# Kernel optimization log

Hardware: AMD Instinct MI355X
Metric: run time of the kernel (lower is better)

## Reference

```python
import math
import jax, jax.numpy as jnp
import numpy as np

N_HEAD = 16
STEP_DIM = 4


def _make_mask(T):
    # lower-triangular causal mask with every STEP_DIM-th column zeroed
    m = jnp.tril(jnp.ones((T, T), dtype=jnp.float32))
    cols = jnp.arange(T)
    keep_col = (cols % STEP_DIM) != (STEP_DIM - 1)
    return m * keep_col[None, :].astype(jnp.float32)  # [T, T]


def setup_inputs() -> dict:
    key = jax.random.key(0)
    ks = jax.random.split(key, 9)
    B, T, C = 2, 2048, 1024
    s = 1.0 / math.sqrt(C)
    return {
        "x": jax.random.normal(ks[0], (B, T, C), dtype=jnp.float32),
        "Wq": jax.random.normal(ks[1], (C, C), dtype=jnp.float32) * s,
        "bq": jnp.zeros((C,), dtype=jnp.float32),
        "Wk": jax.random.normal(ks[2], (C, C), dtype=jnp.float32) * s,
        "bk": jnp.zeros((C,), dtype=jnp.float32),
        "Wv": jax.random.normal(ks[3], (C, C), dtype=jnp.float32) * s,
        "bv": jnp.zeros((C,), dtype=jnp.float32),
        "Wp": jax.random.normal(ks[4], (C, C), dtype=jnp.float32) * s,
        "bp": jnp.zeros((C,), dtype=jnp.float32),
    }


def reference(x, Wq, bq, Wk, bk, Wv, bv, Wp, bp):
    B, T, C = x.shape
    H = N_HEAD
    D = C // H
    # QKV projections -> [B, H, T, D]
    def heads(y):
        return y.reshape(B, T, H, D).transpose(0, 2, 1, 3)
    q = heads(x @ Wq + bq)
    k = heads(x @ Wk + bk)
    v = heads(x @ Wv + bv)
    # scores [B, H, T, T]
    att = jnp.einsum("bhtd,bhsd->bhts", q, k) * (1.0 / math.sqrt(D))
    mask = _make_mask(T)  # [T, T]
    att = jnp.where(mask[None, None, :, :] == 0, -jnp.inf, att)
    att = jax.nn.softmax(att, axis=-1)
    y = jnp.einsum("bhts,bhsd->bhtd", att, v)  # [B, H, T, D]
    y = y.transpose(0, 2, 1, 3).reshape(B, T, C)
    return y @ Wp + bp
```

## Files before the change

### kernel.cpp

```cpp
#include <hip/hip_runtime.h>

typedef __bf16 bf16x8 __attribute__((ext_vector_type(8)));
typedef float  f32x4  __attribute__((ext_vector_type(4)));
typedef unsigned int u32x2 __attribute__((ext_vector_type(2)));
typedef unsigned short u16x8 __attribute__((ext_vector_type(8)));
typedef __attribute__((address_space(3))) const unsigned short* lds_cp;

#define T_SEQ 2048
#define C_DIM 1024
#define NH    16
#define HD    64
#define LOG2E 1.4426950408889634f

__device__ __forceinline__ unsigned short f2bf(float f) {
  unsigned u = __builtin_bit_cast(unsigned, f);
  u += 0x7FFFu + ((u >> 16) & 1u);
  return (unsigned short)(u >> 16);
}

__device__ __forceinline__ unsigned cvtpk(float lo, float hi) {
  unsigned r;
  asm("v_cvt_pk_bf16_f32 %0, %1, %2" : "=v"(r) : "v"(lo), "v"(hi));
  return r;
}

__device__ __forceinline__ bf16x8 tr_frag(lds_cp addr) {
  u32x2 lo, hi;
  asm volatile("ds_read_b64_tr_b16 %0, %2 offset:0\n\t"
               "ds_read_b64_tr_b16 %1, %2 offset:128"
               : "=&v"(lo), "=&v"(hi) : "v"(addr) : "memory");
  struct { u32x2 a, b; } s{lo, hi};
  return __builtin_bit_cast(bf16x8, s);
}

__device__ __forceinline__ void gload_lds16(const void* g, void* l) {
  __builtin_amdgcn_global_load_lds(
      (const __attribute__((address_space(1))) unsigned int*)g,
      (__attribute__((address_space(3))) unsigned int*)l, 16, 0, 0);
}

__global__ void k_cvt_x(const float* __restrict__ x, unsigned short* __restrict__ xb,
                        const float* __restrict__ bq, const float* __restrict__ bk,
                        const float* __restrict__ bv, float* __restrict__ bqkv) {
  const int bx = blockIdx.x;
  if (bx < 4096) {
    const int i = bx * 256 + threadIdx.x;
    const float4 v = ((const float4*)x)[i];
    ushort4 o;
    o.x = f2bf(v.x); o.y = f2bf(v.y); o.z = f2bf(v.z); o.w = f2bf(v.w);
    ((ushort4*)xb)[i] = o;
  } else {
    const int i = (bx - 4096) * 256 + threadIdx.x;
    bqkv[i] = (i < 1024) ? bq[i] : (i < 2048 ? bk[i - 1024] : bv[i - 2048]);
  }
}

__global__ void k_transpose_w(const float* __restrict__ Wq, const float* __restrict__ Wk,
                              const float* __restrict__ Wv, const float* __restrict__ Wp,
                              unsigned short* __restrict__ Wt,
                              unsigned short* __restrict__ Wpt) {
  __shared__ float tile[32][33];
  const int z = blockIdx.z;
  const float* W = (z == 0) ? Wq : (z == 1) ? Wk : (z == 2) ? Wv : Wp;
  unsigned short* D = (z < 3) ? (Wt + ((size_t)z << 20)) : Wpt;
  const int tx = threadIdx.x, ty = threadIdx.y;
  const int n0 = blockIdx.x * 32, k0 = blockIdx.y * 32;
#pragma unroll
  for (int i = 0; i < 32; i += 8)
    tile[ty + i][tx] = W[(size_t)(k0 + ty + i) * C_DIM + n0 + tx];
  __syncthreads();
#pragma unroll
  for (int i = 0; i < 32; i += 8)
    D[(size_t)(n0 + ty + i) * C_DIM + k0 + tx] = f2bf(tile[tx][ty + i]);
}

template<int KDIM>
__device__ __forceinline__ void gemm_tile_mainloop(
    const unsigned short* __restrict__ A,
    const unsigned short* __restrict__ Bt,
    int m0, int n0,
    unsigned short* As, unsigned short* Bs,
    f32x4 acc[4][4])
{
  const int tid  = threadIdx.x;
  const int lane = tid & 63;
  const int wave = tid >> 6;
  const int wr   = wave >> 1, wc = wave & 1;
  const int srow = lane >> 2;
  const int scol = (lane & 3) << 3;
  const int fr   = lane & 15, g = lane >> 4;

  const f32x4 zero = {0.f, 0.f, 0.f, 0.f};
#pragma unroll
  for (int m = 0; m < 4; ++m)
#pragma unroll
    for (int n = 0; n < 4; ++n) acc[m][n] = zero;

  const int nk = KDIM >> 5;
  for (int kt = 0; kt < nk; ++kt) {
    const int kb = kt << 5;
#pragma unroll
    for (int i = 0; i < 2; ++i) {
      const int c   = wave * 2 + i;
      const int row = c * 16 + srow;
      gload_lds16(A  + (size_t)(m0 + row) * KDIM + kb + scol, As + c * 512);
      gload_lds16(Bt + (size_t)(n0 + row) * KDIM + kb + scol, Bs + c * 512);
    }
    __syncthreads();
    bf16x8 af[4], bfr[4];
    const unsigned short* ap = As + (wr * 64 + fr) * 32 + g * 8;
    const unsigned short* bp = Bs + (wc * 64 + fr) * 32 + g * 8;
#pragma unroll
    for (int m = 0; m < 4; ++m) af[m]  = *(const bf16x8*)(ap + m * 512);
#pragma unroll
    for (int n = 0; n < 4; ++n) bfr[n] = *(const bf16x8*)(bp + n * 512);
#pragma unroll
    for (int m = 0; m < 4; ++m)
#pragma unroll
      for (int n = 0; n < 4; ++n)
        acc[m][n] = __builtin_amdgcn_mfma_f32_16x16x32_bf16(af[m], bfr[n], acc[m][n], 0, 0, 0);
    __syncthreads();
  }
}

__global__ __launch_bounds__(256) void k_gemm_qkv(
    const unsigned short* __restrict__ Xb,
    const unsigned short* __restrict__ Wt,
    const float* __restrict__ bias,
    unsigned short* __restrict__ Qb,
    unsigned short* __restrict__ Kb,
    unsigned short* __restrict__ Vt)
{
  __shared__ __attribute__((aligned(16))) unsigned short As[128 * 32];
  __shared__ __attribute__((aligned(16))) unsigned short Bs[128 * 32];
  f32x4 acc[4][4];
  const int bx  = blockIdx.x;
  const int xcd = bx & 7;
  const int jb  = bx >> 3;
  const int m0  = (xcd * 4 + (jb & 3)) * 128;
  const int n0  = (jb >> 2) * 128;
  gemm_tile_mainloop<1024>(Xb, Wt, m0, n0, As, Bs, acc);

  const int lane = threadIdx.x & 63, wave = threadIdx.x >> 6;
  const int wr = wave >> 1, wc = wave & 1;
  const int fr = lane & 15, g = lane >> 4;
  const int j = n0 >> 10;
#pragma unroll
  for (int ni = 0; ni < 4; ++ni) {
    const int col = n0 + wc * 64 + ni * 16 + fr;
    const int c = col & 1023, h = c >> 6, d = c & 63;
    const float bb = bias[col];
#pragma unroll
    for (int mi = 0; mi < 4; ++mi)
#pragma unroll
      for (int r = 0; r < 4; ++r) {
        const int row = m0 + wr * 64 + mi * 16 + g * 4 + r;
        const int b = row >> 11, t = row & 2047;
        const int bh = b * NH + h;
        const float v = acc[mi][ni][r] + bb;
        if (j == 0)      Qb[((size_t)bh * T_SEQ + t) * HD + d] = f2bf(v * (0.125f * LOG2E));
        else if (j == 1) Kb[((size_t)bh * T_SEQ + t) * HD + d] = f2bf(v);
        else             Vt[((size_t)bh * HD + d) * T_SEQ + t] =
                           ((t & 3) == 3) ? (unsigned short)0 : f2bf(v);
      }
  }
}

__global__ __launch_bounds__(128) void k_attn(
    const unsigned short* __restrict__ Qb,
    const unsigned short* __restrict__ Kb,
    const unsigned short* __restrict__ Vt,
    unsigned short* __restrict__ Yb)
{
  __shared__ __attribute__((aligned(128))) unsigned short Ks[2][64][64];
  __shared__ __attribute__((aligned(128))) unsigned short Vs[2][64][64];
  __shared__ __attribute__((aligned(128))) unsigned short Pc[2][2][64][16];

  const int i    = blockIdx.x;
  const int xcd  = i & 7;
  const int jj   = i >> 3;
  const int bh   = xcd * 4 + (jj & 3);
  const int qs   = jj >> 2;
  const int so   = qs >> 3;
  const int qtile = (so == 0) ? 31 - qs : (so == 1) ? qs - 8
                  : (so == 2) ? 39 - qs : qs - 16;
  const int lane  = threadIdx.x & 63;
  const int wave  = threadIdx.x >> 6;
  const int fr = lane & 15, g = lane >> 4;
  const int q0w = qtile * 64 + wave * 32;
  const int nt = qtile + 1;
  const size_t hbase = (size_t)bh * T_SEQ * HD;
  const unsigned short* Kh = Kb + hbase;
  const unsigned short* Vh = Vt + (size_t)bh * HD * T_SEQ;

  const int srow = lane >> 3;
  const int scol = ((lane & 7) ^ srow) << 3;
  const int frx  = (fr & 7) << 3;

  const unsigned short* qp = Qb + hbase + (size_t)(q0w + fr) * HD + g * 8;
  const bf16x8 qA0 = *(const bf16x8*)(qp);
  const bf16x8 qA1 = *(const bf16x8*)(qp + 32);
  const bf16x8 qB0 = *(const bf16x8*)(qp + 16 * HD);
  const bf16x8 qB1 = *(const bf16x8*)(qp + 16 * HD + 32);

  const u16x8 bo = {0x3F80u, 0x3F80u, 0x3F80u, 0u, 0x3F80u, 0x3F80u, 0x3F80u, 0u};
  const bf16x8 bones = __builtin_bit_cast(bf16x8, bo);

  const f32x4 zero = {0.f, 0.f, 0.f, 0.f};
  f32x4 yA[4], yB[4], lAcc, lBcc;
#pragma unroll
  for (int n = 0; n < 4; ++n) { yA[n] = zero; yB[n] = zero; }
  lAcc = zero; lBcc = zero;

  char* pwA = (char*)&Pc[wave][0][0][0] + fr * 32 + g * 8;
  char* pwB = (char*)&Pc[wave][1][0][0] + fr * 32 + g * 8;
  lds_cp trA = (lds_cp)(const unsigned short*)&Pc[wave][0][0][0] + fr * 4 + g * 128;
  lds_cp trB = (lds_cp)(const unsigned short*)&Pc[wave][1][0][0] + fr * 4 + g * 128;

  auto STAGE = [&](int buf, int s0) {
#pragma unroll
    for (int i2 = 0; i2 < 4; ++i2) {
      const int c = wave * 4 + i2;
      gload_lds16(Kh + (size_t)(s0 + c * 8 + srow) * HD + scol, &Ks[buf][c * 8][0]);
      gload_lds16(Vh + (size_t)(c * 8 + srow) * T_SEQ + s0 + scol, &Vs[buf][c * 8][0]);
    }
  };

  auto BODY = [&](int cur, int s0, bool diag) {
    bf16x8 kf[4][2];
#pragma unroll
    for (int n = 0; n < 4; ++n) {
      const unsigned short* kr = &Ks[cur][n * 16 + fr][0];
      kf[n][0] = *(const bf16x8*)(kr + ((g * 8) ^ frx));
      kf[n][1] = *(const bf16x8*)(kr + ((32 + g * 8) ^ frx));
    }
    f32x4 sA[4], sB[4];
#pragma unroll
    for (int n = 0; n < 4; ++n) {
      f32x4 a = zero, b = zero;
      a = __builtin_amdgcn_mfma_f32_16x16x32_bf16(qA0, kf[n][0], a, 0, 0, 0);
      a = __builtin_amdgcn_mfma_f32_16x16x32_bf16(qA1, kf[n][1], a, 0, 0, 0);
      b = __builtin_amdgcn_mfma_f32_16x16x32_bf16(qB0, kf[n][0], b, 0, 0, 0);
      b = __builtin_amdgcn_mfma_f32_16x16x32_bf16(qB1, kf[n][1], b, 0, 0, 0);
      sA[n] = a; sB[n] = b;
    }
    if (diag) {
#pragma unroll
      for (int n = 0; n < 4; ++n) {
        const int sc = s0 + n * 16 + fr;
#pragma unroll
        for (int r = 0; r < 4; ++r) {
          const int tA = q0w + g * 4 + r;
          sA[n][r] = (sc <= tA) ? sA[n][r] : -1e30f;
          sB[n][r] = (sc <= tA + 16) ? sB[n][r] : -1e30f;
        }
      }
    }
    bf16x8 vf[4][2];
#pragma unroll
    for (int n = 0; n < 4; ++n) {
      const unsigned short* vr = &Vs[cur][n * 16 + fr][0];
      vf[n][0] = *(const bf16x8*)(vr + ((g * 8) ^ frx));
      vf[n][1] = *(const bf16x8*)(vr + ((32 + g * 8) ^ frx));
    }
#pragma unroll
    for (int n = 0; n < 4; ++n) {
      u32x2 wa = {cvtpk(exp2f(sA[n][0]), exp2f(sA[n][1])),
                  cvtpk(exp2f(sA[n][2]), exp2f(sA[n][3]))};
      u32x2 wb = {cvtpk(exp2f(sB[n][0]), exp2f(sB[n][1])),
                  cvtpk(exp2f(sB[n][2]), exp2f(sB[n][3]))};
      *(u32x2*)(pwA + n * 512) = wa;
      *(u32x2*)(pwB + n * 512) = wb;
    }
    bf16x8 paA[2], paB[2];
    paA[0] = tr_frag(trA);       paA[1] = tr_frag(trA + 512);
    paB[0] = tr_frag(trB);       paB[1] = tr_frag(trB + 512);
    asm volatile("s_waitcnt lgkmcnt(0)" ::: "memory");
    __builtin_amdgcn_sched_barrier(0);
#pragma unroll
    for (int kk = 0; kk < 2; ++kk) {
#pragma unroll
      for (int n = 0; n < 4; ++n) {
        yA[n] = __builtin_amdgcn_mfma_f32_16x16x32_bf16(paA[kk], vf[n][kk], yA[n], 0, 0, 0);
        yB[n] = __builtin_amdgcn_mfma_f32_16x16x32_bf16(paB[kk], vf[n][kk], yB[n], 0, 0, 0);
      }
      lAcc = __builtin_amdgcn_mfma_f32_16x16x32_bf16(paA[kk], bones, lAcc, 0, 0, 0);
      lBcc = __builtin_amdgcn_mfma_f32_16x16x32_bf16(paB[kk], bones, lBcc, 0, 0, 0);
    }
  };

  STAGE(0, 0);
  __syncthreads();
  for (int t = 0; t < nt; ++t) {
    const int cur = t & 1;
    if (t + 1 < nt) STAGE(cur ^ 1, (t + 1) * 64);
    const int s0 = t * 64;
    BODY(cur, s0, s0 + 63 > q0w);
    __syncthreads();
  }

  const int b = bh >> 4, h = bh & 15;
#pragma unroll
  for (int r = 0; r < 4; ++r) {
    const float invA = 1.0f / lAcc[r], invB = 1.0f / lBcc[r];
    const int tA = q0w + g * 4 + r;
#pragma unroll
    for (int n = 0; n < 4; ++n) {
      Yb[((size_t)(b * T_SEQ + tA)) * C_DIM + h * HD + n * 16 + fr] = f2bf(yA[n][r] * invA);
      Yb[((size_t)(b * T_SEQ + tA + 16)) * C_DIM + h * HD + n * 16 + fr] = f2bf(yB[n][r] * invB);
    }
  }
}

__global__ __launch_bounds__(256) void k_gemm_out(
    const unsigned short* __restrict__ Yb,
    const unsigned short* __restrict__ Wpt,
    const float* __restrict__ bp,
    float* __restrict__ out)
{
  __shared__ __attribute__((aligned(16))) unsigned short As[128 * 32];
  __shared__ __attribute__((aligned(16))) unsigned short Bs[128 * 32];
  f32x4 acc[4][4];
  const int bx  = blockIdx.x;
  const int xcd = bx & 7;
  const int jb  = bx >> 3;
  const int m0  = (xcd * 4 + (jb & 3)) * 128;
  const int n0  = (jb >> 2) * 128;
  gemm_tile_mainloop<1024>(Yb, Wpt, m0, n0, As, Bs, acc);

  const int lane = threadIdx.x & 63, wave = threadIdx.x >> 6;
  const int wr = wave >> 1, wc = wave & 1;
  const int fr = lane & 15, g = lane >> 4;
#pragma unroll
  for (int ni = 0; ni < 4; ++ni) {
    const int col = n0 + wc * 64 + ni * 16 + fr;
    const float bb = bp[col];
#pragma unroll
    for (int mi = 0; mi < 4; ++mi)
#pragma unroll
      for (int r = 0; r < 4; ++r) {
        const int row = m0 + wr * 64 + mi * 16 + g * 4 + r;
        out[(size_t)row * C_DIM + col] = acc[mi][ni][r] + bb;
      }
  }
}

extern "C" void kernel_launch(void* const* d_in, const int* in_sizes, int n_in,
                              void* d_out, int out_size, void* d_ws, size_t ws_size,
                              hipStream_t stream) {
  const float* x  = (const float*)d_in[0];
  const float* Wq = (const float*)d_in[1];
  const float* bq = (const float*)d_in[2];
  const float* Wk = (const float*)d_in[3];
  const float* bk = (const float*)d_in[4];
  const float* Wv = (const float*)d_in[5];
  const float* bv = (const float*)d_in[6];
  const float* Wp = (const float*)d_in[7];
  const float* bp = (const float*)d_in[8];
  float* out = (float*)d_out;

  char* ws = (char*)d_ws;
  unsigned short* Xb   = (unsigned short*)(ws);
  unsigned short* Wt   = (unsigned short*)(ws + (8u  << 20));
  unsigned short* Wpt  = (unsigned short*)(ws + (14u << 20));
  float*          bqkv = (float*)         (ws + (16u << 20));
  unsigned short* Qb   = (unsigned short*)(ws + (16u << 20) + (64u << 10));
  unsigned short* Kb   = (unsigned short*)(ws + (24u << 20) + (64u << 10));
  unsigned short* Vt   = (unsigned short*)(ws + (32u << 20) + (64u << 10));
  unsigned short* Yb   = (unsigned short*)(ws + (40u << 20) + (64u << 10));

  k_cvt_x<<<4108, 256, 0, stream>>>(x, Xb, bq, bk, bv, bqkv);
  dim3 tb(32, 8);
  k_transpose_w<<<dim3(32, 32, 4), tb, 0, stream>>>(Wq, Wk, Wv, Wp, Wt, Wpt);
  k_gemm_qkv<<<dim3(768), 256, 0, stream>>>(Xb, Wt, bqkv, Qb, Kb, Vt);
  k_attn<<<dim3(1024), 128, 0, stream>>>(Qb, Kb, Vt, Yb);
  k_gemm_out<<<dim3(256), 256, 0, stream>>>(Yb, Wpt, bp, out);
}
```

Before: 130.9 us.

## Split long causal attention tiles across two KV halves and merge partials

Query tiles 16-31 are now processed by two blocks each, one per half of the KV range. Each block writes unnormalized fp32 partial outputs and row sums, and a new merge kernel adds the two partials and normalizes. The goal is to balance per-block work under the causal mask, so a few long tiles no longer set the tail. In exchange it adds an extra kernel launch, fp32 partial traffic to global memory, and relies on no running max being subtracted, so the partial sums can be added directly.

```diff
diff --git a/kernel.cpp b/kernel.cpp
--- a/kernel.cpp
+++ b/kernel.cpp
@@ -170,7 +170,9 @@
     const unsigned short* __restrict__ Qb,
     const unsigned short* __restrict__ Kb,
     const unsigned short* __restrict__ Vt,
-    unsigned short* __restrict__ Yb)
+    unsigned short* __restrict__ Yb,
+    float* __restrict__ Ypart,
+    float* __restrict__ Lpart)
 {
   __shared__ __attribute__((aligned(128))) unsigned short Ks[2][64][64];
   __shared__ __attribute__((aligned(128))) unsigned short Vs[2][64][64];
@@ -178,17 +180,20 @@
 
   const int i    = blockIdx.x;
   const int xcd  = i & 7;
-  const int jj   = i >> 3;
-  const int bh   = xcd * 4 + (jj & 3);
-  const int qs   = jj >> 2;
-  const int so   = qs >> 3;
-  const int qtile = (so == 0) ? 31 - qs : (so == 1) ? qs - 8
-                  : (so == 2) ? 39 - qs : qs - 16;
+  const int j    = i >> 3;
+  const int bh   = xcd * 4 + (j & 3);
+  const int u    = j >> 2;
+  const int gg   = u >> 3, vv0 = u & 7;
+  const int vv   = (gg & 1) ? 7 - vv0 : vv0;
+  int qtile, t0, t1, half;
+  if (gg < 2)      { qtile = (gg == 0 ? 16 : 24) + vv; t0 = 0; t1 = (qtile + 1) >> 1; half = 0; }
+  else if (gg < 4) { qtile = (gg == 2 ? 16 : 24) + vv; t0 = (qtile + 1) >> 1; t1 = qtile + 1; half = 1; }
+  else             { qtile = (gg == 4 ? 0 : 8) + vv;   t0 = 0; t1 = qtile + 1; half = -1; }
+
   const int lane  = threadIdx.x & 63;
   const int wave  = threadIdx.x >> 6;
   const int fr = lane & 15, g = lane >> 4;
   const int q0w = qtile * 64 + wave * 32;
-  const int nt = qtile + 1;
   const size_t hbase = (size_t)bh * T_SEQ * HD;
   const unsigned short* Kh = Kb + hbase;
   const unsigned short* Vh = Vt + (size_t)bh * HD * T_SEQ;
@@ -289,27 +294,58 @@
     }
   };
 
-  STAGE(0, 0);
+  STAGE(0, t0 * 64);
   __syncthreads();
-  for (int t = 0; t < nt; ++t) {
-    const int cur = t & 1;
-    if (t + 1 < nt) STAGE(cur ^ 1, (t + 1) * 64);
+  for (int t = t0; t < t1; ++t) {
+    const int cur = (t - t0) & 1;
+    if (t + 1 < t1) STAGE(cur ^ 1, (t + 1) * 64);
     const int s0 = t * 64;
     BODY(cur, s0, s0 + 63 > q0w);
     __syncthreads();
   }
 
+  if (half < 0) {
+    const int b = bh >> 4, h = bh & 15;
+#pragma unroll
+    for (int r = 0; r < 4; ++r) {
+      const float invA = 1.0f / lAcc[r], invB = 1.0f / lBcc[r];
+      const int tA = q0w + g * 4 + r;
+#pragma unroll
+      for (int n = 0; n < 4; ++n) {
+        Yb[((size_t)(b * T_SEQ + tA)) * C_DIM + h * HD + n * 16 + fr] = f2bf(yA[n][r] * invA);
+        Yb[((size_t)(b * T_SEQ + tA + 16)) * C_DIM + h * HD + n * 16 + fr] = f2bf(yB[n][r] * invB);
+      }
+    }
+  } else {
+    float* Yp = Ypart + (((size_t)half * 32 + bh) << 16);
+    float* Lp = Lpart + (((size_t)half * 32 + bh) << 10);
+    const int rb = (qtile - 16) * 64 + wave * 32;
+#pragma unroll
+    for (int r = 0; r < 4; ++r) {
+      const int rowA = rb + g * 4 + r, rowB = rowA + 16;
+#pragma unroll
+      for (int n = 0; n < 4; ++n) {
+        Yp[rowA * 64 + n * 16 + fr] = yA[n][r];
+        Yp[rowB * 64 + n * 16 + fr] = yB[n][r];
+      }
+      if (fr == 0) { Lp[rowA] = lAcc[r]; Lp[rowB] = lBcc[r]; }
+    }
+  }
+}
+
+__global__ __launch_bounds__(256) void k_merge(
+    const float* __restrict__ Ypart, const float* __restrict__ Lpart,
+    unsigned short* __restrict__ Yb)
+{
+  const int idx = blockIdx.x * 256 + threadIdx.x;
+  const int d   = idx & 63;
+  const int row = (idx >> 6) & 1023;
+  const int bh  = idx >> 16;
+  const size_t o0 = ((size_t)bh << 16) + row * 64 + d;
+  const float y = Ypart[o0] + Ypart[(32ull << 16) + o0];
+  const float l = Lpart[((size_t)bh << 10) + row] + Lpart[(32ull << 10) + ((size_t)bh << 10) + row];
   const int b = bh >> 4, h = bh & 15;
-#pragma unroll
-  for (int r = 0; r < 4; ++r) {
-    const float invA = 1.0f / lAcc[r], invB = 1.0f / lBcc[r];
-    const int tA = q0w + g * 4 + r;
-#pragma unroll
-    for (int n = 0; n < 4; ++n) {
-      Yb[((size_t)(b * T_SEQ + tA)) * C_DIM + h * HD + n * 16 + fr] = f2bf(yA[n][r] * invA);
-      Yb[((size_t)(b * T_SEQ + tA + 16)) * C_DIM + h * HD + n * 16 + fr] = f2bf(yB[n][r] * invB);
-    }
-  }
+  Yb[((size_t)(b * T_SEQ + 1024 + row)) * C_DIM + h * HD + d] = f2bf(y / l);
 }
 
 __global__ __launch_bounds__(256) void k_gemm_out(
@@ -368,11 +404,14 @@
   unsigned short* Kb   = (unsigned short*)(ws + (24u << 20) + (64u << 10));
   unsigned short* Vt   = (unsigned short*)(ws + (32u << 20) + (64u << 10));
   unsigned short* Yb   = (unsigned short*)(ws + (40u << 20) + (64u << 10));
+  float*          Yp   = (float*)         (ws + (48u << 20) + (64u << 10));
+  float*          Lp   = (float*)         (ws + (64u << 20) + (64u << 10));
 
   k_cvt_x<<<4108, 256, 0, stream>>>(x, Xb, bq, bk, bv, bqkv);
   dim3 tb(32, 8);
   k_transpose_w<<<dim3(32, 32, 4), tb, 0, stream>>>(Wq, Wk, Wv, Wp, Wt, Wpt);
   k_gemm_qkv<<<dim3(768), 256, 0, stream>>>(Xb, Wt, bqkv, Qb, Kb, Vt);
-  k_attn<<<dim3(1024), 128, 0, stream>>>(Qb, Kb, Vt, Yb);
+  k_attn<<<dim3(1536), 128, 0, stream>>>(Qb, Kb, Vt, Yb, Yp, Lp);
+  k_merge<<<dim3(8192), 256, 0, stream>>>(Yp, Lp, Yb);
   k_gemm_out<<<dim3(256), 256, 0, stream>>>(Yb, Wpt, bp, out);
 }
```

Measured after the change: 134.2 us. 2.6% more time.

## Halve attention query tile per block, load V fragments straight from global

Applied to the files above, without the earlier changes.

Each attention block now handles 32 query rows (16 per wave) instead of 64, which doubles the grid to 2048 blocks and uses a new zig-zag mapping of blocks to query tiles for load balance. V is no longer staged in LDS; each wave reads its V fragments directly from global memory every iteration. The shared-memory footprint and register use drop, and launch bounds ask for 4 blocks per CU to raise occupancy. In exchange, K tiles are reloaded for twice as many blocks and the uncoalesced global V reads could add latency.

```diff
diff --git a/kernel.cpp b/kernel.cpp
--- a/kernel.cpp
+++ b/kernel.cpp
@@ -166,29 +166,29 @@
   }
 }
 
-__global__ __launch_bounds__(128) void k_attn(
+__global__ __launch_bounds__(128, 4) void k_attn(
     const unsigned short* __restrict__ Qb,
     const unsigned short* __restrict__ Kb,
     const unsigned short* __restrict__ Vt,
     unsigned short* __restrict__ Yb)
 {
   __shared__ __attribute__((aligned(128))) unsigned short Ks[2][64][64];
-  __shared__ __attribute__((aligned(128))) unsigned short Vs[2][64][64];
-  __shared__ __attribute__((aligned(128))) unsigned short Pc[2][2][64][16];
+  __shared__ __attribute__((aligned(128))) unsigned short Pc[2][64][16];
 
   const int i    = blockIdx.x;
   const int xcd  = i & 7;
   const int jj   = i >> 3;
   const int bh   = xcd * 4 + (jj & 3);
-  const int qs   = jj >> 2;
-  const int so   = qs >> 3;
-  const int qtile = (so == 0) ? 31 - qs : (so == 1) ? qs - 8
-                  : (so == 2) ? 39 - qs : qs - 16;
-  const int lane  = threadIdx.x & 63;
-  const int wave  = threadIdx.x >> 6;
+  const int u    = jj >> 2;
+  const int g8   = u >> 3, v8 = u & 7;
+  const int w8   = (g8 & 1) ? 7 - v8 : v8;
+  const int qt   = 63 - (g8 + 8 * w8);
+  const int lane = threadIdx.x & 63;
+  const int wave = threadIdx.x >> 6;
   const int fr = lane & 15, g = lane >> 4;
-  const int q0w = qtile * 64 + wave * 32;
-  const int nt = qtile + 1;
+  const int q0w = qt * 32 + wave * 16;
+  const int ndiag = qt >> 1;
+  const int nt = ndiag + 1;
   const size_t hbase = (size_t)bh * T_SEQ * HD;
   const unsigned short* Kh = Kb + hbase;
   const unsigned short* Vh = Vt + (size_t)bh * HD * T_SEQ;
@@ -200,33 +200,28 @@
   const unsigned short* qp = Qb + hbase + (size_t)(q0w + fr) * HD + g * 8;
   const bf16x8 qA0 = *(const bf16x8*)(qp);
   const bf16x8 qA1 = *(const bf16x8*)(qp + 32);
-  const bf16x8 qB0 = *(const bf16x8*)(qp + 16 * HD);
-  const bf16x8 qB1 = *(const bf16x8*)(qp + 16 * HD + 32);
 
   const u16x8 bo = {0x3F80u, 0x3F80u, 0x3F80u, 0u, 0x3F80u, 0x3F80u, 0x3F80u, 0u};
   const bf16x8 bones = __builtin_bit_cast(bf16x8, bo);
 
   const f32x4 zero = {0.f, 0.f, 0.f, 0.f};
-  f32x4 yA[4], yB[4], lAcc, lBcc;
-#pragma unroll
-  for (int n = 0; n < 4; ++n) { yA[n] = zero; yB[n] = zero; }
-  lAcc = zero; lBcc = zero;
-
-  char* pwA = (char*)&Pc[wave][0][0][0] + fr * 32 + g * 8;
-  char* pwB = (char*)&Pc[wave][1][0][0] + fr * 32 + g * 8;
-  lds_cp trA = (lds_cp)(const unsigned short*)&Pc[wave][0][0][0] + fr * 4 + g * 128;
-  lds_cp trB = (lds_cp)(const unsigned short*)&Pc[wave][1][0][0] + fr * 4 + g * 128;
+  f32x4 yA[4], lAcc;
+#pragma unroll
+  for (int n = 0; n < 4; ++n) yA[n] = zero;
+  lAcc = zero;
+
+  char* pwA = (char*)&Pc[wave][0][0] + fr * 32 + g * 8;
+  lds_cp trA = (lds_cp)(const unsigned short*)&Pc[wave][0][0] + fr * 4 + g * 128;
 
   auto STAGE = [&](int buf, int s0) {
 #pragma unroll
     for (int i2 = 0; i2 < 4; ++i2) {
       const int c = wave * 4 + i2;
       gload_lds16(Kh + (size_t)(s0 + c * 8 + srow) * HD + scol, &Ks[buf][c * 8][0]);
-      gload_lds16(Vh + (size_t)(c * 8 + srow) * T_SEQ + s0 + scol, &Vs[buf][c * 8][0]);
     }
   };
 
-  auto BODY = [&](int cur, int s0, bool diag) {
+  auto BODY = [&](int cur, int s0, bool diag, const bf16x8 (&vf)[4][2]) {
     bf16x8 kf[4][2];
 #pragma unroll
     for (int n = 0; n < 4; ++n) {
@@ -234,15 +229,13 @@
       kf[n][0] = *(const bf16x8*)(kr + ((g * 8) ^ frx));
       kf[n][1] = *(const bf16x8*)(kr + ((32 + g * 8) ^ frx));
     }
-    f32x4 sA[4], sB[4];
+    f32x4 sA[4];
 #pragma unroll
     for (int n = 0; n < 4; ++n) {
-      f32x4 a = zero, b = zero;
+      f32x4 a = zero;
       a = __builtin_amdgcn_mfma_f32_16x16x32_bf16(qA0, kf[n][0], a, 0, 0, 0);
       a = __builtin_amdgcn_mfma_f32_16x16x32_bf16(qA1, kf[n][1], a, 0, 0, 0);
-      b = __builtin_amdgcn_mfma_f32_16x16x32_bf16(qB0, kf[n][0], b, 0, 0, 0);
-      b = __builtin_amdgcn_mfma_f32_16x16x32_bf16(qB1, kf[n][1], b, 0, 0, 0);
-      sA[n] = a; sB[n] = b;
+      sA[n] = a;
     }
     if (diag) {
 #pragma unroll
@@ -252,40 +245,25 @@
         for (int r = 0; r < 4; ++r) {
           const int tA = q0w + g * 4 + r;
           sA[n][r] = (sc <= tA) ? sA[n][r] : -1e30f;
-          sB[n][r] = (sc <= tA + 16) ? sB[n][r] : -1e30f;
         }
       }
-    }
-    bf16x8 vf[4][2];
-#pragma unroll
-    for (int n = 0; n < 4; ++n) {
-      const unsigned short* vr = &Vs[cur][n * 16 + fr][0];
-      vf[n][0] = *(const bf16x8*)(vr + ((g * 8) ^ frx));
-      vf[n][1] = *(const bf16x8*)(vr + ((32 + g * 8) ^ frx));
     }
 #pragma unroll
     for (int n = 0; n < 4; ++n) {
       u32x2 wa = {cvtpk(exp2f(sA[n][0]), exp2f(sA[n][1])),
                   cvtpk(exp2f(sA[n][2]), exp2f(sA[n][3]))};
-      u32x2 wb = {cvtpk(exp2f(sB[n][0]), exp2f(sB[n][1])),
-                  cvtpk(exp2f(sB[n][2]), exp2f(sB[n][3]))};
       *(u32x2*)(pwA + n * 512) = wa;
-      *(u32x2*)(pwB + n * 512) = wb;
-    }
-    bf16x8 paA[2], paB[2];
+    }
+    bf16x8 paA[2];
     paA[0] = tr_frag(trA);       paA[1] = tr_frag(trA + 512);
-    paB[0] = tr_frag(trB);       paB[1] = tr_frag(trB + 512);
     asm volatile("s_waitcnt lgkmcnt(0)" ::: "memory");
     __builtin_amdgcn_sched_barrier(0);
 #pragma unroll
     for (int kk = 0; kk < 2; ++kk) {
 #pragma unroll
-      for (int n = 0; n < 4; ++n) {
+      for (int n = 0; n < 4; ++n)
         yA[n] = __builtin_amdgcn_mfma_f32_16x16x32_bf16(paA[kk], vf[n][kk], yA[n], 0, 0, 0);
-        yB[n] = __builtin_amdgcn_mfma_f32_16x16x32_bf16(paB[kk], vf[n][kk], yB[n], 0, 0, 0);
-      }
       lAcc = __builtin_amdgcn_mfma_f32_16x16x32_bf16(paA[kk], bones, lAcc, 0, 0, 0);
-      lBcc = __builtin_amdgcn_mfma_f32_16x16x32_bf16(paB[kk], bones, lBcc, 0, 0, 0);
     }
   };
 
@@ -293,22 +271,26 @@
   __syncthreads();
   for (int t = 0; t < nt; ++t) {
     const int cur = t & 1;
+    const int s0 = t * 64;
+    bf16x8 vf[4][2];
+#pragma unroll
+    for (int n = 0; n < 4; ++n)
+#pragma unroll
+      for (int kk = 0; kk < 2; ++kk)
+        vf[n][kk] = *(const bf16x8*)(Vh + (size_t)(n * 16 + fr) * T_SEQ + s0 + kk * 32 + g * 8);
     if (t + 1 < nt) STAGE(cur ^ 1, (t + 1) * 64);
-    const int s0 = t * 64;
-    BODY(cur, s0, s0 + 63 > q0w);
+    BODY(cur, s0, s0 + 63 > q0w, vf);
     __syncthreads();
   }
 
   const int b = bh >> 4, h = bh & 15;
 #pragma unroll
   for (int r = 0; r < 4; ++r) {
-    const float invA = 1.0f / lAcc[r], invB = 1.0f / lBcc[r];
+    const float invA = 1.0f / lAcc[r];
     const int tA = q0w + g * 4 + r;
 #pragma unroll
-    for (int n = 0; n < 4; ++n) {
+    for (int n = 0; n < 4; ++n)
       Yb[((size_t)(b * T_SEQ + tA)) * C_DIM + h * HD + n * 16 + fr] = f2bf(yA[n][r] * invA);
-      Yb[((size_t)(b * T_SEQ + tA + 16)) * C_DIM + h * HD + n * 16 + fr] = f2bf(yB[n][r] * invB);
-    }
   }
 }
 
@@ -373,6 +355,6 @@
   dim3 tb(32, 8);
   k_transpose_w<<<dim3(32, 32, 4), tb, 0, stream>>>(Wq, Wk, Wv, Wp, Wt, Wpt);
   k_gemm_qkv<<<dim3(768), 256, 0, stream>>>(Xb, Wt, bqkv, Qb, Kb, Vt);
-  k_attn<<<dim3(1024), 128, 0, stream>>>(Qb, Kb, Vt, Yb);
+  k_attn<<<dim3(2048), 128, 0, stream>>>(Qb, Kb, Vt, Yb);
   k_gemm_out<<<dim3(256), 256, 0, stream>>>(Yb, Wpt, bp, out);
 }
```

After: 148.4 us. 13.4% more time.

## Software-pipeline attention PV MFMAs behind next QK and merge prep kernels

Applied to the files above, without the earlier changes.

The attention loop is restructured so the P·V MFMAs for the previous tile are issued after the current tile's QK^T MFMAs. This lets the exp/convert and LDS round trip of P overlap with matrix work, and the V fragments are carried across iterations in registers with a drain step after the loop. The next K/V tile is now staged later, after the current V reads, which shortens the prefetch window. The x conversion and weight transpose kernels are also fused into one launch to remove a kernel launch gap, at the cost of more register pressure in the attention kernel.

```diff
diff --git a/kernel.cpp b/kernel.cpp
--- a/kernel.cpp
+++ b/kernel.cpp
@@ -39,9 +39,14 @@
       (__attribute__((address_space(3))) unsigned int*)l, 16, 0, 0);
 }
 
-__global__ void k_cvt_x(const float* __restrict__ x, unsigned short* __restrict__ xb,
-                        const float* __restrict__ bq, const float* __restrict__ bk,
-                        const float* __restrict__ bv, float* __restrict__ bqkv) {
+__global__ void k_prep(const float* __restrict__ x, unsigned short* __restrict__ xb,
+                       const float* __restrict__ bq, const float* __restrict__ bk,
+                       const float* __restrict__ bv, float* __restrict__ bqkv,
+                       const float* __restrict__ Wq, const float* __restrict__ Wk,
+                       const float* __restrict__ Wv, const float* __restrict__ Wp,
+                       unsigned short* __restrict__ Wt,
+                       unsigned short* __restrict__ Wpt) {
+  __shared__ float tile[32][33];
   const int bx = blockIdx.x;
   if (bx < 4096) {
     const int i = bx * 256 + threadIdx.x;
@@ -49,29 +54,25 @@
     ushort4 o;
     o.x = f2bf(v.x); o.y = f2bf(v.y); o.z = f2bf(v.z); o.w = f2bf(v.w);
     ((ushort4*)xb)[i] = o;
-  } else {
+  } else if (bx < 4108) {
     const int i = (bx - 4096) * 256 + threadIdx.x;
     bqkv[i] = (i < 1024) ? bq[i] : (i < 2048 ? bk[i - 1024] : bv[i - 2048]);
-  }
-}
-
-__global__ void k_transpose_w(const float* __restrict__ Wq, const float* __restrict__ Wk,
-                              const float* __restrict__ Wv, const float* __restrict__ Wp,
-                              unsigned short* __restrict__ Wt,
-                              unsigned short* __restrict__ Wpt) {
-  __shared__ float tile[32][33];
-  const int z = blockIdx.z;
-  const float* W = (z == 0) ? Wq : (z == 1) ? Wk : (z == 2) ? Wv : Wp;
-  unsigned short* D = (z < 3) ? (Wt + ((size_t)z << 20)) : Wpt;
-  const int tx = threadIdx.x, ty = threadIdx.y;
-  const int n0 = blockIdx.x * 32, k0 = blockIdx.y * 32;
-#pragma unroll
-  for (int i = 0; i < 32; i += 8)
-    tile[ty + i][tx] = W[(size_t)(k0 + ty + i) * C_DIM + n0 + tx];
-  __syncthreads();
-#pragma unroll
-  for (int i = 0; i < 32; i += 8)
-    D[(size_t)(n0 + ty + i) * C_DIM + k0 + tx] = f2bf(tile[tx][ty + i]);
+  } else {
+    const int bi  = bx - 4108;
+    const int z   = bi >> 10;
+    const int idx = bi & 1023;
+    const int n0  = (idx & 31) * 32, k0 = (idx >> 5) * 32;
+    const float* W = (z == 0) ? Wq : (z == 1) ? Wk : (z == 2) ? Wv : Wp;
+    unsigned short* D = (z < 3) ? (Wt + ((size_t)z << 20)) : Wpt;
+    const int tx = threadIdx.x & 31, ty = threadIdx.x >> 5;
+#pragma unroll
+    for (int i = 0; i < 32; i += 8)
+      tile[ty + i][tx] = W[(size_t)(k0 + ty + i) * C_DIM + n0 + tx];
+    __syncthreads();
+#pragma unroll
+    for (int i = 0; i < 32; i += 8)
+      D[(size_t)(n0 + ty + i) * C_DIM + k0 + tx] = f2bf(tile[tx][ty + i]);
+  }
 }
 
 template<int KDIM>
@@ -211,6 +212,7 @@
 #pragma unroll
   for (int n = 0; n < 4; ++n) { yA[n] = zero; yB[n] = zero; }
   lAcc = zero; lBcc = zero;
+  bf16x8 vfOld[4][2];
 
   char* pwA = (char*)&Pc[wave][0][0][0] + fr * 32 + g * 8;
   char* pwB = (char*)&Pc[wave][1][0][0] + fr * 32 + g * 8;
@@ -226,7 +228,12 @@
     }
   };
 
-  auto BODY = [&](int cur, int s0, bool diag) {
+  STAGE(0, 0);
+  __syncthreads();
+  for (int t = 0; t < nt; ++t) {
+    const int cur = t & 1;
+    const int s0 = t * 64;
+    const bool diag = (s0 + 63 > q0w);
     bf16x8 kf[4][2];
 #pragma unroll
     for (int n = 0; n < 4; ++n) {
@@ -234,6 +241,13 @@
       kf[n][0] = *(const bf16x8*)(kr + ((g * 8) ^ frx));
       kf[n][1] = *(const bf16x8*)(kr + ((32 + g * 8) ^ frx));
     }
+    bf16x8 paA[2], paB[2];
+    if (t > 0) {
+      paA[0] = tr_frag(trA);  paA[1] = tr_frag(trA + 512);
+      paB[0] = tr_frag(trB);  paB[1] = tr_frag(trB + 512);
+    }
+    asm volatile("s_waitcnt lgkmcnt(0)" ::: "memory");
+    __builtin_amdgcn_sched_barrier(0);
     f32x4 sA[4], sB[4];
 #pragma unroll
     for (int n = 0; n < 4; ++n) {
@@ -244,6 +258,18 @@
       b = __builtin_amdgcn_mfma_f32_16x16x32_bf16(qB1, kf[n][1], b, 0, 0, 0);
       sA[n] = a; sB[n] = b;
     }
+    if (t > 0) {
+#pragma unroll
+      for (int kk = 0; kk < 2; ++kk) {
+#pragma unroll
+        for (int n = 0; n < 4; ++n) {
+          yA[n] = __builtin_amdgcn_mfma_f32_16x16x32_bf16(paA[kk], vfOld[n][kk], yA[n], 0, 0, 0);
+          yB[n] = __builtin_amdgcn_mfma_f32_16x16x32_bf16(paB[kk], vfOld[n][kk], yB[n], 0, 0, 0);
+        }
+        lAcc = __builtin_amdgcn_mfma_f32_16x16x32_bf16(paA[kk], bones, lAcc, 0, 0, 0);
+        lBcc = __builtin_amdgcn_mfma_f32_16x16x32_bf16(paB[kk], bones, lBcc, 0, 0, 0);
+      }
+    }
     if (diag) {
 #pragma unroll
       for (int n = 0; n < 4; ++n) {
@@ -255,13 +281,6 @@
           sB[n][r] = (sc <= tA + 16) ? sB[n][r] : -1e30f;
         }
       }
-    }
-    bf16x8 vf[4][2];
-#pragma unroll
-    for (int n = 0; n < 4; ++n) {
-      const unsigned short* vr = &Vs[cur][n * 16 + fr][0];
-      vf[n][0] = *(const bf16x8*)(vr + ((g * 8) ^ frx));
-      vf[n][1] = *(const bf16x8*)(vr + ((32 + g * 8) ^ frx));
     }
 #pragma unroll
     for (int n = 0; n < 4; ++n) {
@@ -272,31 +291,31 @@
       *(u32x2*)(pwA + n * 512) = wa;
       *(u32x2*)(pwB + n * 512) = wb;
     }
+#pragma unroll
+    for (int n = 0; n < 4; ++n) {
+      const unsigned short* vr = &Vs[cur][n * 16 + fr][0];
+      vfOld[n][0] = *(const bf16x8*)(vr + ((g * 8) ^ frx));
+      vfOld[n][1] = *(const bf16x8*)(vr + ((32 + g * 8) ^ frx));
+    }
+    if (t + 1 < nt) STAGE(cur ^ 1, (t + 1) * 64);
+    __syncthreads();
+  }
+  {
     bf16x8 paA[2], paB[2];
-    paA[0] = tr_frag(trA);       paA[1] = tr_frag(trA + 512);
-    paB[0] = tr_frag(trB);       paB[1] = tr_frag(trB + 512);
+    paA[0] = tr_frag(trA);  paA[1] = tr_frag(trA + 512);
+    paB[0] = tr_frag(trB);  paB[1] = tr_frag(trB + 512);
     asm volatile("s_waitcnt lgkmcnt(0)" ::: "memory");
     __builtin_amdgcn_sched_barrier(0);
 #pragma unroll
     for (int kk = 0; kk < 2; ++kk) {
 #pragma unroll
       for (int n = 0; n < 4; ++n) {
-        yA[n] = __builtin_amdgcn_mfma_f32_16x16x32_bf16(paA[kk], vf[n][kk], yA[n], 0, 0, 0);
-        yB[n] = __builtin_amdgcn_mfma_f32_16x16x32_bf16(paB[kk], vf[n][kk], yB[n], 0, 0, 0);
+        yA[n] = __builtin_amdgcn_mfma_f32_16x16x32_bf16(paA[kk], vfOld[n][kk], yA[n], 0, 0, 0);
+        yB[n] = __builtin_amdgcn_mfma_f32_16x16x32_bf16(paB[kk], vfOld[n][kk], yB[n], 0, 0, 0);
       }
       lAcc = __builtin_amdgcn_mfma_f32_16x16x32_bf16(paA[kk], bones, lAcc, 0, 0, 0);
       lBcc = __builtin_amdgcn_mfma_f32_16x16x32_bf16(paB[kk], bones, lBcc, 0, 0, 0);
     }
-  };
-
-  STAGE(0, 0);
-  __syncthreads();
-  for (int t = 0; t < nt; ++t) {
-    const int cur = t & 1;
-    if (t + 1 < nt) STAGE(cur ^ 1, (t + 1) * 64);
-    const int s0 = t * 64;
-    BODY(cur, s0, s0 + 63 > q0w);
-    __syncthreads();
   }
 
   const int b = bh >> 4, h = bh & 15;
@@ -369,9 +388,7 @@
   unsigned short* Vt   = (unsigned short*)(ws + (32u << 20) + (64u << 10));
   unsigned short* Yb   = (unsigned short*)(ws + (40u << 20) + (64u << 10));
 
-  k_cvt_x<<<4108, 256, 0, stream>>>(x, Xb, bq, bk, bv, bqkv);
-  dim3 tb(32, 8);
-  k_transpose_w<<<dim3(32, 32, 4), tb, 0, stream>>>(Wq, Wk, Wv, Wp, Wt, Wpt);
+  k_prep<<<8204, 256, 0, stream>>>(x, Xb, bq, bk, bv, bqkv, Wq, Wk, Wv, Wp, Wt, Wpt);
   k_gemm_qkv<<<dim3(768), 256, 0, stream>>>(Xb, Wt, bqkv, Qb, Kb, Vt);
   k_attn<<<dim3(1024), 128, 0, stream>>>(Qb, Kb, Vt, Yb);
   k_gemm_out<<<dim3(256), 256, 0, stream>>>(Yb, Wpt, bp, out);
```

After: 121.4 us. 1.08x faster.
